# Kernel optimization log

Measured on AMD Instinct MI355X. Metric: run time of the kernel, lower is better.

Reference implementation:

```python
import jax, jax.numpy as jnp
import numpy as np

N, D, W, S = 16384, 256, 64, 8  # utterances, embed dim, attention half-window, speakers


def setup_inputs() -> dict:
    key = jax.random.key(0)
    ks = jax.random.split(key, 8)
    scale = 1.0 / np.sqrt(D)
    return {
        "x": jax.random.normal(ks[0], (N, D), jnp.float32),
        "speaker_ids": jax.random.randint(ks[1], (N,), 0, S, jnp.int32),
        "W_att": jax.random.normal(ks[2], (D, D), jnp.float32) * scale,
        "W_pred": jax.random.normal(ks[3], (D, D), jnp.float32) * scale,
        "W_suc": jax.random.normal(ks[4], (D, D), jnp.float32) * scale,
        "W_same": jax.random.normal(ks[5], (D, D), jnp.float32) * scale,
        "W_diff": jax.random.normal(ks[6], (D, D), jnp.float32) * scale,
    }


def reference(x, speaker_ids, W_att, W_pred, W_suc, W_same, W_diff):
    n = x.shape[0]
    pad = jnp.zeros((W, D), x.dtype)
    # windowed gather: for utterance i, neighbors at offsets [-W, W-1] (2W slots)
    win_idx = jnp.arange(n)[:, None] + jnp.arange(2 * W)[None, :]  # index into padded [N+2W]
    xp = jnp.concatenate([pad, x, pad], axis=0)                    # [N+2W, D]
    windows = xp[win_idx]                                          # [N, 2W, D]
    # raw_attn[i,w] = (edge_att_weights(windows[i,w])) . x[i]
    raw_attn = jnp.einsum("nwd,ed,ne->nw", windows, W_att, x)      # [N, 2W]
    attn = jax.nn.softmax(raw_attn, axis=1)
    # relation masks over the band: j = i + offset
    offs = jnp.arange(2 * W) - W                                   # [-W, W-1]
    j = jnp.arange(n)[:, None] + offs[None, :]                     # [N, 2W]
    valid = (j >= 0) & (j < n)
    jc = jnp.clip(j, 0, n - 1)
    same_spk = speaker_ids[jc] == speaker_ids[:, None]
    masks = [
        valid & (offs >= 0)[None, :],   # pred: edges to current/future within window
        valid & (offs < 0)[None, :],    # suc: edges to past within window
        valid & same_spk,               # same speaker within window
        valid & ~same_spk,              # different speaker within window
    ]
    # relation-specific GCN aggregation: h = sum_r A_r @ (x @ W_r), A_r banded
    h = jnp.zeros_like(x)
    for Wr, m in zip([W_pred, W_suc, W_same, W_diff], masks):
        support = x @ Wr                                           # [N, D]
        sp = jnp.concatenate([pad, support, pad], axis=0)[win_idx]  # [N, 2W, D]
        h = h + jnp.einsum("nw,nwd->nd", attn * m, sp)
    return jax.nn.log_softmax(h, axis=1)
```

## Files before the change

kernel.cpp:

```cpp
#include <hip/hip_runtime.h>
#include <hip/hip_bf16.h>

typedef unsigned short u16;
typedef unsigned int u32;
typedef __attribute__((ext_vector_type(8))) short short8;
typedef __attribute__((ext_vector_type(4))) float floatx4;

#define NU 16384
#define DIM 256
#define AMS 200
#define AC1o 6400u
#define FYLO 8448u

#define XHo 0u
#define XLo 4194304u
#define XRo 8388608u
#define ST0 20971520u
#define STROW 16512u
#define STMAT 4227072u
#define WH0o 33652736u
#define WL0o 33718272u
#define WRo  33783808u

__device__ __forceinline__ u16 bfh(float v) {
  return (u16)(__float_as_uint(v) >> 16);
}
__device__ __forceinline__ float bup(u16 u) {
  return __uint_as_float(((u32)u) << 16);
}
__device__ __forceinline__ u16 bfrn(float v) {
  u32 u = __float_as_uint(v);
  return (u16)((u + 0x7fffu + ((u >> 16) & 1u)) >> 16);
}

__global__ __launch_bounds__(256) void prep(
    const float* __restrict__ x,
    const float* __restrict__ wat, const float* __restrict__ wpr,
    const float* __restrict__ wsu, const float* __restrict__ wsm,
    const float* __restrict__ wdf, u16* __restrict__ ws) {
  const int b = blockIdx.x, t = threadIdx.x;
  if (b < 2048) {
    int idx = (b * 256 + t) * 8;
    float4 v0 = *(const float4*)(x + idx);
    float4 v1 = *(const float4*)(x + idx + 4);
    float a[8] = {v0.x, v0.y, v0.z, v0.w, v1.x, v1.y, v1.z, v1.w};
    u16 h[8], l[8], r[8];
#pragma unroll
    for (int q = 0; q < 8; ++q) {
      h[q] = bfh(a[q]);
      l[q] = bfh(a[q] - bup(h[q]));
      r[q] = bfrn(a[q]);
    }
    *(uint4*)(ws + XHo + idx) = *(const uint4*)h;
    *(uint4*)(ws + XLo + idx) = *(const uint4*)l;
    *(uint4*)(ws + XRo + idx) = *(const uint4*)r;
    return;
  }
  const int b2 = b - 2048;
  if (b2 < 32) {
    const int s = b2 & 7, mat = b2 >> 3, n = t;
    const float* Wa = (mat == 0) ? wat : (mat == 1) ? wpr : (mat == 2) ? wsm : wsu;
    const float* Wb = (mat == 0) ? wat : (mat == 1) ? wsu : (mat == 2) ? wdf : wdf;
    const float c1  = (mat == 0) ? 0.f : (mat == 3) ? 1.f : -1.f;
    u16 hbuf[32], lbuf[32];
#pragma unroll 8
    for (int k = 0; k < 32; ++k) {
      float v = Wa[(s * 32 + k) * 256 + n] + c1 * Wb[(s * 32 + k) * 256 + n];
      if (mat == 0) { hbuf[k] = bfh(v); lbuf[k] = bfh(v - bup(hbuf[k])); }
      else          { hbuf[k] = bfrn(v); }
    }
    u16* dh = ws + ((mat == 0) ? WH0o : (WRo + (size_t)(mat - 1) * 65536))
               + (size_t)s * 8192 + n * 32;
#pragma unroll
    for (int p = 0; p < 4; ++p) *(uint4*)(dh + p * 8) = ((const uint4*)hbuf)[p];
    if (mat == 0) {
      u16* dl = ws + WL0o + (size_t)s * 8192 + n * 32;
#pragma unroll
      for (int p = 0; p < 4; ++p) *(uint4*)(dl + p * 8) = ((const uint4*)lbuf)[p];
    }
  } else {
    int g = (b2 - 32) * 256 + t;
    int r = g >> 13, rem = g & 8191;
    int d = rem >> 5, p = rem & 31;
    size_t base = ST0 + (size_t)r * STMAT + (size_t)d * STROW;
    size_t off = (p < 16) ? (base + p * 4) : (base + 16448 + (p - 16) * 4);
    *(ushort4*)(ws + off) = make_ushort4(0, 0, 0, 0);
  }
}

__global__ __launch_bounds__(512, 4) void gemmS1(u16* __restrict__ ws) {
  __shared__ __align__(16) u16 U[39168];

  const int t = threadIdx.x, row0 = blockIdx.x * 32;
  const int w = t >> 6, ln = t & 15, quad = (t & 63) >> 4, q8 = quad * 8;
  const int n0 = w * 32;

#pragma unroll
  for (int cc = 0; cc < 2; ++cc) {
    int idx = t + 512 * cc;
    int row = idx >> 5, c8 = (idx & 31) * 8;
    *(uint4*)(U + row * 264 + c8) =
        *(const uint4*)(ws + XRo + (size_t)(row0 + row) * 256 + c8);
  }
  __syncthreads();

  floatx4 acc[3][2][2];
#pragma unroll
  for (int mat = 0; mat < 3; ++mat)
#pragma unroll
    for (int m = 0; m < 2; ++m)
#pragma unroll
      for (int nt = 0; nt < 2; ++nt) acc[mat][m][nt] = (floatx4){0.f, 0.f, 0.f, 0.f};

  for (int s = 0; s < 8; ++s) {
    short8 ah[2];
#pragma unroll
    for (int m = 0; m < 2; ++m)
      ah[m] = *(const short8*)(U + (m * 16 + ln) * 264 + s * 32 + q8);
#pragma unroll
    for (int mat = 0; mat < 3; ++mat) {
      short8 bh[2];
#pragma unroll
      for (int nt = 0; nt < 2; ++nt)
        bh[nt] = *(const short8*)(ws + WRo + (size_t)mat * 65536
                                  + (size_t)s * 8192 + (n0 + nt * 16 + ln) * 32 + q8);
#pragma unroll
      for (int m = 0; m < 2; ++m)
#pragma unroll
        for (int nt = 0; nt < 2; ++nt)
          acc[mat][m][nt] = __builtin_amdgcn_mfma_f32_16x16x32_bf16(ah[m], bh[nt], acc[mat][m][nt], 0, 0, 0);
    }
  }

#pragma unroll
  for (int mat = 0; mat < 3; ++mat)
#pragma unroll
    for (int m = 0; m < 2; ++m)
#pragma unroll
      for (int nt = 0; nt < 2; ++nt) {
        int col = n0 + nt * 16 + ln;
        ushort4 pk = make_ushort4(bfrn(acc[mat][m][nt][0]), bfrn(acc[mat][m][nt][1]),
                                  bfrn(acc[mat][m][nt][2]), bfrn(acc[mat][m][nt][3]));
        *(ushort4*)(U + 8448 + mat * 10240 + col * 40 + m * 16 + quad * 4) = pk;
      }
  __syncthreads();

#pragma unroll
  for (int mat = 0; mat < 3; ++mat)
#pragma unroll
    for (int cc = 0; cc < 2; ++cc) {
      int c = t + 512 * cc;
      int d = c >> 2, part = c & 3;
      *(uint4*)(ws + ST0 + (size_t)mat * STMAT + (size_t)d * STROW + 64 + row0 + part * 8) =
          *(const uint4*)(U + 8448 + mat * 10240 + d * 40 + part * 8);
    }
}

__global__ __launch_bounds__(512, 4) void fused_attn(
    const u16* __restrict__ ws, const int* __restrict__ spk,
    float* __restrict__ out)
{
  __shared__ __align__(16) u16 U[16896];
  __shared__ int spkw[192];
  __shared__ float prt[32][4], prs[32][4];
  __shared__ float red[32][8];

  const int t    = threadIdx.x;
  const int w    = t >> 6;
  const int ln   = t & 15;
  const int quad = (t & 63) >> 4;
  const int q8   = quad * 8;
  const int bswz = (blockIdx.x & 7) * 64 + (blockIdx.x >> 3);
  const int i0   = bswz * 32;
  const int mw   = w & 1;
  const int wq   = w >> 1;
  const int n0   = w * 32;

  if (t < 192) spkw[t] = spk[min(max(i0 - 64 + t, 0), NU - 1)];

  {
#pragma unroll
    for (int cc = 0; cc < 4; ++cc) {
      int idx = t + 512 * cc;
      int buf = idx >> 10, e = idx & 1023;
      int row = e >> 5, c8 = (e & 31) * 8;
      *(uint4*)(U + buf * FYLO + row * 264 + c8) =
          *(const uint4*)(ws + (buf ? XLo : XHo) + (size_t)(i0 + row) * 256 + c8);
    }
    __syncthreads();

    floatx4 acc[2][2];
#pragma unroll
    for (int m = 0; m < 2; ++m)
#pragma unroll
      for (int nt = 0; nt < 2; ++nt) acc[m][nt] = (floatx4){0.f, 0.f, 0.f, 0.f};

    for (int s = 0; s < 8; ++s) {
      short8 ah[2], al[2];
#pragma unroll
      for (int m = 0; m < 2; ++m) {
        ah[m] = *(const short8*)(U + (m * 16 + ln) * 264 + s * 32 + q8);
        al[m] = *(const short8*)(U + FYLO + (m * 16 + ln) * 264 + s * 32 + q8);
      }
      short8 bh[2], bl[2];
#pragma unroll
      for (int nt = 0; nt < 2; ++nt) {
        size_t off = (size_t)s * 8192 + (n0 + nt * 16 + ln) * 32 + q8;
        bh[nt] = *(const short8*)(ws + WH0o + off);
        bl[nt] = *(const short8*)(ws + WL0o + off);
      }
#pragma unroll
      for (int m = 0; m < 2; ++m)
#pragma unroll
        for (int nt = 0; nt < 2; ++nt) {
          acc[m][nt] = __builtin_amdgcn_mfma_f32_16x16x32_bf16(ah[m], bh[nt], acc[m][nt], 0, 0, 0);
          acc[m][nt] = __builtin_amdgcn_mfma_f32_16x16x32_bf16(ah[m], bl[nt], acc[m][nt], 0, 0, 0);
          acc[m][nt] = __builtin_amdgcn_mfma_f32_16x16x32_bf16(al[m], bh[nt], acc[m][nt], 0, 0, 0);
        }
    }
    __syncthreads();

#pragma unroll
    for (int m = 0; m < 2; ++m)
#pragma unroll
      for (int nt = 0; nt < 2; ++nt) {
        int col = n0 + nt * 16 + ln;
#pragma unroll
        for (int r = 0; r < 4; ++r) {
          int row = m * 16 + quad * 4 + r;
          float y = acc[m][nt][r];
          u16 hh = bfh(y);
          U[row * 264 + col] = hh;
          U[FYLO + row * 264 + col] = bfh(y - bup(hh));
        }
      }
  }
  __syncthreads();

  floatx4 accP[3];
#pragma unroll
  for (int cc = 0; cc < 3; ++cc) accP[cc] = (floatx4){0.f, 0.f, 0.f, 0.f};

#pragma unroll 2
  for (int ks = 0; ks < 8; ++ks) {
    const u16* yb = U + (mw * 16 + ln) * 264 + ks * 32 + q8;
    short8 yh8 = *(const short8*)yb;
    short8 yl8 = *(const short8*)(yb + FYLO);
#pragma unroll
    for (int cc = 0; cc < 3; ++cc) {
      int xrow = wq * 48 + cc * 16 + ln;
      int jc = min(max(i0 + xrow - 64, 0), NU - 1);
      size_t xo = (size_t)jc * 256 + ks * 32 + q8;
      short8 xbh = *(const short8*)(ws + XHo + xo);
      short8 xbl = *(const short8*)(ws + XLo + xo);
      accP[cc] = __builtin_amdgcn_mfma_f32_16x16x32_bf16(yh8, xbh, accP[cc], 0, 0, 0);
      accP[cc] = __builtin_amdgcn_mfma_f32_16x16x32_bf16(yh8, xbl, accP[cc], 0, 0, 0);
      accP[cc] = __builtin_amdgcn_mfma_f32_16x16x32_bf16(yl8, xbh, accP[cc], 0, 0, 0);
    }
  }

  int  c_of[3];
  bool vj[3];
#pragma unroll
  for (int cc = 0; cc < 3; ++cc) {
    c_of[cc] = wq * 48 + cc * 16 + ln;
    int j = i0 + c_of[cc] - 64;
    vj[cc] = (j >= 0) && (j < NU);
  }
#pragma unroll
  for (int r = 0; r < 4; ++r) {
    int row = mw * 16 + quad * 4 + r;
    float mx = -3.4e38f;
#pragma unroll
    for (int cc = 0; cc < 3; ++cc) {
      int rel = c_of[cc] - row;
      bool inb = (rel >= 0) && (rel < 128);
      if (inb) mx = fmaxf(mx, vj[cc] ? accP[cc][r] : 0.f);
    }
#pragma unroll
    for (int o = 1; o < 16; o <<= 1) mx = fmaxf(mx, __shfl_xor(mx, o));
    if (ln == 0) prt[row][wq] = mx;
  }
  __syncthreads();
#pragma unroll
  for (int r = 0; r < 4; ++r) {
    int row = mw * 16 + quad * 4 + r;
    float gm = fmaxf(fmaxf(prt[row][0], prt[row][1]), fmaxf(prt[row][2], prt[row][3]));
    float s = 0.f;
#pragma unroll
    for (int cc = 0; cc < 3; ++cc) {
      int rel = c_of[cc] - row;
      bool inb = (rel >= 0) && (rel < 128);
      float vv = vj[cc] ? accP[cc][r] : 0.f;
      float e  = inb ? __expf(vv - gm) : 0.f;
      s += e;
      accP[cc][r] = (inb && vj[cc]) ? e : 0.f;
    }
#pragma unroll
    for (int o = 1; o < 16; o <<= 1) s += __shfl_xor(s, o);
    if (ln == 0) prs[row][wq] = s;
  }
  __syncthreads();
#pragma unroll
  for (int r = 0; r < 4; ++r) {
    int row = mw * 16 + quad * 4 + r;
    float inv = 1.f / (prs[row][0] + prs[row][1] + prs[row][2] + prs[row][3]);
#pragma unroll
    for (int cc = 0; cc < 3; ++cc)
      U[row * AMS + c_of[cc]] = bfrn(accP[cc][r] * inv);
  }
  __syncthreads();

  {
    const int arow = t >> 4, aseg = t & 15;
    const int sr = spkw[arow + 64];
    const int cb = aseg * 12;
#pragma unroll
    for (int p = 0; p < 3; ++p) {
      ushort4 av = *(const ushort4*)(U + arow * AMS + cb + p * 4);
      u16 aq[4] = {av.x, av.y, av.z, av.w};
      u16 b1v[4];
#pragma unroll
      for (int q = 0; q < 4; ++q) {
        int c = cb + p * 4 + q;
        b1v[q] = (spkw[c] == sr) ? aq[q] : (u16)0;
      }
      *(ushort4*)(U + AC1o + arow * AMS + cb + p * 4) = *(const ushort4*)b1v;
    }
  }
  __syncthreads();

  floatx4 acc2[2][2];
#pragma unroll
  for (int m = 0; m < 2; ++m)
#pragma unroll
    for (int nt = 0; nt < 2; ++nt) acc2[m][nt] = (floatx4){0.f, 0.f, 0.f, 0.f};

#pragma unroll
  for (int kj = 0; kj < 5; ++kj) {
    short8 af[2], af1[2];
#pragma unroll
    for (int m = 0; m < 2; ++m) {
      af[m]  = *(const short8*)(U + (m * 16 + ln) * AMS + kj * 32 + q8);
      af1[m] = *(const short8*)(U + AC1o + (m * 16 + ln) * AMS + kj * 32 + q8);
    }
    size_t sb[2];
#pragma unroll
    for (int nt = 0; nt < 2; ++nt)
      sb[nt] = (size_t)ST0 + (size_t)(n0 + nt * 16 + ln) * STROW
             + (size_t)(i0 + kj * 32) + q8;
#pragma unroll
    for (int nt = 0; nt < 2; ++nt) {
      short8 b2 = *(const short8*)(ws + sb[nt] + 2 * (size_t)STMAT);
      short8 b1 = *(const short8*)(ws + sb[nt] + 1 * (size_t)STMAT);
#pragma unroll
      for (int m = 0; m < 2; ++m) {
        acc2[m][nt] = __builtin_amdgcn_mfma_f32_16x16x32_bf16(af[m],  b2, acc2[m][nt], 0, 0, 0);
        acc2[m][nt] = __builtin_amdgcn_mfma_f32_16x16x32_bf16(af1[m], b1, acc2[m][nt], 0, 0, 0);
      }
    }
    if (kj >= 2) {
      short8 a0m[2];
#pragma unroll
      for (int m = 0; m < 2; ++m) {
        a0m[m] = af[m];
        if (!(32 * kj >= 16 * m + 79)) {
          int tthr = m * 16 + ln + 64 - kj * 32 - q8;
#pragma unroll
          for (int e = 0; e < 8; ++e)
            if (e < tthr) a0m[m][e] = 0;
        }
      }
#pragma unroll
      for (int nt = 0; nt < 2; ++nt) {
        short8 b0 = *(const short8*)(ws + sb[nt]);
#pragma unroll
        for (int m = 0; m < 2; ++m) {
          if (32 * kj < 16 * m + 33) continue;
          acc2[m][nt] = __builtin_amdgcn_mfma_f32_16x16x32_bf16(a0m[m], b0, acc2[m][nt], 0, 0, 0);
        }
      }
    }
  }

#pragma unroll
  for (int m = 0; m < 2; ++m)
#pragma unroll
    for (int r = 0; r < 4; ++r) {
      float v = fmaxf(acc2[m][0][r], acc2[m][1][r]);
#pragma unroll
      for (int o = 1; o < 16; o <<= 1) v = fmaxf(v, __shfl_xor(v, o));
      if (ln == 0) red[m * 16 + quad * 4 + r][w] = v;
    }
  __syncthreads();
  float gmx[2][4];
#pragma unroll
  for (int m = 0; m < 2; ++m)
#pragma unroll
    for (int r = 0; r < 4; ++r) {
      int row = m * 16 + quad * 4 + r;
      float g = red[row][0];
#pragma unroll
      for (int ww = 1; ww < 8; ++ww) g = fmaxf(g, red[row][ww]);
      gmx[m][r] = g;
    }
  __syncthreads();
#pragma unroll
  for (int m = 0; m < 2; ++m)
#pragma unroll
    for (int r = 0; r < 4; ++r) {
      float e = __expf(acc2[m][0][r] - gmx[m][r]) + __expf(acc2[m][1][r] - gmx[m][r]);
#pragma unroll
      for (int o = 1; o < 16; o <<= 1) e += __shfl_xor(e, o);
      if (ln == 0) red[m * 16 + quad * 4 + r][w] = e;
    }
  __syncthreads();
#pragma unroll
  for (int m = 0; m < 2; ++m)
#pragma unroll
    for (int r = 0; r < 4; ++r) {
      int row = m * 16 + quad * 4 + r;
      float s = red[row][0];
#pragma unroll
      for (int ww = 1; ww < 8; ++ww) s += red[row][ww];
      float lse = gmx[m][r] + logf(s);
      size_t rowg = (size_t)(i0 + row) * DIM;
      out[rowg + n0 + ln]      = acc2[m][0][r] - lse;
      out[rowg + n0 + 16 + ln] = acc2[m][1][r] - lse;
    }
}

extern "C" void kernel_launch(void* const* d_in, const int* in_sizes, int n_in,
                              void* d_out, int out_size, void* d_ws, size_t ws_size,
                              hipStream_t stream) {
  const float* x   = (const float*)d_in[0];
  const int*   spk = (const int*)d_in[1];
  const float* wat = (const float*)d_in[2];
  const float* wpr = (const float*)d_in[3];
  const float* wsu = (const float*)d_in[4];
  const float* wsm = (const float*)d_in[5];
  const float* wdf = (const float*)d_in[6];
  float* out = (float*)d_out;
  u16* ws = (u16*)d_ws;

  hipLaunchKernelGGL(prep, dim3(2176), dim3(256), 0, stream,
                     x, wat, wpr, wsu, wsm, wdf, ws);
  hipLaunchKernelGGL(gemmS1, dim3(512), dim3(512), 0, stream, ws);
  hipLaunchKernelGGL(fused_attn, dim3(512), dim3(512), 0, stream, ws, spk, out);
}
```

Baseline: 161.3 us.

## Stage neighbor X tiles in LDS with double-buffered async loads; drop XR copy

The attention-score GEMM used to read the neighbor rows of X straight from global memory for every wave. Now a 160-row window of hi/lo bf16 X is staged into LDS with global_load_lds, double-buffered across the k-steps, using an XOR swizzle to spread bank accesses. The wave-to-column split is rebalanced to cover 160 columns (3+3+2+2 tiles) instead of 192, which removes redundant out-of-band work. gemmS1 now converts fp32 x to bf16 itself, so prep no longer writes the rounded copy. The trade-off is a larger LDS footprint with occupancy reduced to 2 blocks per CU, plus a barrier on every k-step.

```diff
diff --git a/kernel.cpp b/kernel.cpp
--- a/kernel.cpp
+++ b/kernel.cpp
@@ -9,12 +9,12 @@
 #define NU 16384
 #define DIM 256
 #define AMS 200
-#define AC1o 6400u
+#define AC1w 6400u
 #define FYLO 8448u
+#define STG32o 16896u
 
 #define XHo 0u
 #define XLo 4194304u
-#define XRo 8388608u
 #define ST0 20971520u
 #define STROW 16512u
 #define STMAT 4227072u
@@ -31,6 +31,12 @@
 __device__ __forceinline__ u16 bfrn(float v) {
   u32 u = __float_as_uint(v);
   return (u16)((u + 0x7fffu + ((u >> 16) & 1u)) >> 16);
+}
+
+__device__ __forceinline__ void gload16(const u16* g, u16* l) {
+  __builtin_amdgcn_global_load_lds(
+      (__attribute__((address_space(1))) void*)(uintptr_t)g,
+      (__attribute__((address_space(3))) void*)(uintptr_t)l, 16, 0, 0);
 }
 
 __global__ __launch_bounds__(256) void prep(
@@ -44,16 +50,14 @@
     float4 v0 = *(const float4*)(x + idx);
     float4 v1 = *(const float4*)(x + idx + 4);
     float a[8] = {v0.x, v0.y, v0.z, v0.w, v1.x, v1.y, v1.z, v1.w};
-    u16 h[8], l[8], r[8];
+    u16 h[8], l[8];
 #pragma unroll
     for (int q = 0; q < 8; ++q) {
       h[q] = bfh(a[q]);
       l[q] = bfh(a[q] - bup(h[q]));
-      r[q] = bfrn(a[q]);
     }
     *(uint4*)(ws + XHo + idx) = *(const uint4*)h;
     *(uint4*)(ws + XLo + idx) = *(const uint4*)l;
-    *(uint4*)(ws + XRo + idx) = *(const uint4*)r;
     return;
   }
   const int b2 = b - 2048;
@@ -88,7 +92,8 @@
   }
 }
 
-__global__ __launch_bounds__(512, 4) void gemmS1(u16* __restrict__ ws) {
+__global__ __launch_bounds__(512, 4) void gemmS1(const float* __restrict__ x,
+                                                 u16* __restrict__ ws) {
   __shared__ __align__(16) u16 U[39168];
 
   const int t = threadIdx.x, row0 = blockIdx.x * 32;
@@ -96,11 +101,12 @@
   const int n0 = w * 32;
 
 #pragma unroll
-  for (int cc = 0; cc < 2; ++cc) {
+  for (int cc = 0; cc < 4; ++cc) {
     int idx = t + 512 * cc;
-    int row = idx >> 5, c8 = (idx & 31) * 8;
-    *(uint4*)(U + row * 264 + c8) =
-        *(const uint4*)(ws + XRo + (size_t)(row0 + row) * 256 + c8);
+    int row = idx >> 6, c4 = (idx & 63) * 4;
+    float4 v = *(const float4*)(x + (size_t)(row0 + row) * 256 + c4);
+    ushort4 pk = make_ushort4(bfrn(v.x), bfrn(v.y), bfrn(v.z), bfrn(v.w));
+    *(ushort4*)(U + row * 264 + c4) = pk;
   }
   __syncthreads();
 
@@ -156,12 +162,12 @@
     }
 }
 
-__global__ __launch_bounds__(512, 4) void fused_attn(
+__global__ __launch_bounds__(512, 2) void fused_attn(
     const u16* __restrict__ ws, const int* __restrict__ spk,
     float* __restrict__ out)
 {
-  __shared__ __align__(16) u16 U[16896];
-  __shared__ int spkw[192];
+  __shared__ __align__(16) u16 U[37376];
+  __shared__ int spkw[160];
   __shared__ float prt[32][4], prs[32][4];
   __shared__ float red[32][8];
 
@@ -173,10 +179,12 @@
   const int bswz = (blockIdx.x & 7) * 64 + (blockIdx.x >> 3);
   const int i0   = bswz * 32;
   const int mw   = w & 1;
-  const int wq   = w >> 1;
+  const int wg   = w >> 1;
+  const int gbase = (wg < 2) ? wg * 48 : 96 + (wg - 2) * 32;
+  const int gcnt  = (wg < 2) ? 3 : 2;
   const int n0   = w * 32;
 
-  if (t < 192) spkw[t] = spk[min(max(i0 - 64 + t, 0), NU - 1)];
+  if (t < 160) spkw[t] = spk[min(max(i0 - 64 + t, 0), NU - 1)];
 
   {
 #pragma unroll
@@ -235,35 +243,59 @@
         }
       }
   }
-  __syncthreads();
+
+  auto STAGE = [&](int ks, int par) {
+    const int kd = ks * 32;
+    u16* db = U + STG32o + par * 10240;
+#pragma unroll
+    for (int cc = 0; cc < 3; ++cc) {
+      int idx = t + 512 * cc;
+      if (idx < 1280) {
+        int bsel = (idx >= 640) ? 1 : 0;
+        int e    = idx - bsel * 640;
+        int row  = e >> 2, s2 = e & 3;
+        int sw   = s2 ^ ((row >> 1) & 3);
+        int jc   = min(max(i0 + row - 64, 0), NU - 1);
+        gload16(ws + (bsel ? XLo : XHo) + (size_t)jc * 256 + kd + sw * 8,
+                db + bsel * 5120 + e * 8);
+      }
+    }
+  };
 
   floatx4 accP[3];
 #pragma unroll
   for (int cc = 0; cc < 3; ++cc) accP[cc] = (floatx4){0.f, 0.f, 0.f, 0.f};
 
-#pragma unroll 2
+  STAGE(0, 0);
+  __syncthreads();
+#pragma unroll
   for (int ks = 0; ks < 8; ++ks) {
+    if (ks < 7) STAGE(ks + 1, (ks + 1) & 1);
+    const u16* sp = U + STG32o + (ks & 1) * 10240;
     const u16* yb = U + (mw * 16 + ln) * 264 + ks * 32 + q8;
     short8 yh8 = *(const short8*)yb;
     short8 yl8 = *(const short8*)(yb + FYLO);
 #pragma unroll
     for (int cc = 0; cc < 3; ++cc) {
-      int xrow = wq * 48 + cc * 16 + ln;
-      int jc = min(max(i0 + xrow - 64, 0), NU - 1);
-      size_t xo = (size_t)jc * 256 + ks * 32 + q8;
-      short8 xbh = *(const short8*)(ws + XHo + xo);
-      short8 xbl = *(const short8*)(ws + XLo + xo);
-      accP[cc] = __builtin_amdgcn_mfma_f32_16x16x32_bf16(yh8, xbh, accP[cc], 0, 0, 0);
-      accP[cc] = __builtin_amdgcn_mfma_f32_16x16x32_bf16(yh8, xbl, accP[cc], 0, 0, 0);
-      accP[cc] = __builtin_amdgcn_mfma_f32_16x16x32_bf16(yl8, xbh, accP[cc], 0, 0, 0);
-    }
+      if (cc < gcnt) {
+        int xrow = gbase + cc * 16 + ln;
+        int slot = quad ^ ((xrow >> 1) & 3);
+        const u16* xb = sp + xrow * 32 + slot * 8;
+        short8 xbh = *(const short8*)xb;
+        short8 xbl = *(const short8*)(xb + 5120);
+        accP[cc] = __builtin_amdgcn_mfma_f32_16x16x32_bf16(yh8, xbh, accP[cc], 0, 0, 0);
+        accP[cc] = __builtin_amdgcn_mfma_f32_16x16x32_bf16(yh8, xbl, accP[cc], 0, 0, 0);
+        accP[cc] = __builtin_amdgcn_mfma_f32_16x16x32_bf16(yl8, xbh, accP[cc], 0, 0, 0);
+      }
+    }
+    __syncthreads();
   }
 
   int  c_of[3];
   bool vj[3];
 #pragma unroll
   for (int cc = 0; cc < 3; ++cc) {
-    c_of[cc] = wq * 48 + cc * 16 + ln;
+    c_of[cc] = gbase + cc * 16 + ln;
     int j = i0 + c_of[cc] - 64;
     vj[cc] = (j >= 0) && (j < NU);
   }
@@ -273,13 +305,15 @@
     float mx = -3.4e38f;
 #pragma unroll
     for (int cc = 0; cc < 3; ++cc) {
-      int rel = c_of[cc] - row;
-      bool inb = (rel >= 0) && (rel < 128);
-      if (inb) mx = fmaxf(mx, vj[cc] ? accP[cc][r] : 0.f);
+      if (cc < gcnt) {
+        int rel = c_of[cc] - row;
+        bool inb = (rel >= 0) && (rel < 128);
+        if (inb) mx = fmaxf(mx, vj[cc] ? accP[cc][r] : 0.f);
+      }
     }
 #pragma unroll
     for (int o = 1; o < 16; o <<= 1) mx = fmaxf(mx, __shfl_xor(mx, o));
-    if (ln == 0) prt[row][wq] = mx;
+    if (ln == 0) prt[row][wg] = mx;
   }
   __syncthreads();
 #pragma unroll
@@ -289,16 +323,18 @@
     float s = 0.f;
 #pragma unroll
     for (int cc = 0; cc < 3; ++cc) {
-      int rel = c_of[cc] - row;
-      bool inb = (rel >= 0) && (rel < 128);
-      float vv = vj[cc] ? accP[cc][r] : 0.f;
-      float e  = inb ? __expf(vv - gm) : 0.f;
-      s += e;
-      accP[cc][r] = (inb && vj[cc]) ? e : 0.f;
+      if (cc < gcnt) {
+        int rel = c_of[cc] - row;
+        bool inb = (rel >= 0) && (rel < 128);
+        float vv = vj[cc] ? accP[cc][r] : 0.f;
+        float e  = inb ? __expf(vv - gm) : 0.f;
+        s += e;
+        accP[cc][r] = (inb && vj[cc]) ? e : 0.f;
+      }
     }
 #pragma unroll
     for (int o = 1; o < 16; o <<= 1) s += __shfl_xor(s, o);
-    if (ln == 0) prs[row][wq] = s;
+    if (ln == 0) prs[row][wg] = s;
   }
   __syncthreads();
 #pragma unroll
@@ -307,25 +343,20 @@
     float inv = 1.f / (prs[row][0] + prs[row][1] + prs[row][2] + prs[row][3]);
 #pragma unroll
     for (int cc = 0; cc < 3; ++cc)
-      U[row * AMS + c_of[cc]] = bfrn(accP[cc][r] * inv);
+      if (cc < gcnt)
+        U[row * AMS + c_of[cc]] = bfrn(accP[cc][r] * inv);
   }
   __syncthreads();
 
   {
     const int arow = t >> 4, aseg = t & 15;
     const int sr = spkw[arow + 64];
-    const int cb = aseg * 12;
-#pragma unroll
-    for (int p = 0; p < 3; ++p) {
-      ushort4 av = *(const ushort4*)(U + arow * AMS + cb + p * 4);
-      u16 aq[4] = {av.x, av.y, av.z, av.w};
-      u16 b1v[4];
-#pragma unroll
-      for (int q = 0; q < 4; ++q) {
-        int c = cb + p * 4 + q;
-        b1v[q] = (spkw[c] == sr) ? aq[q] : (u16)0;
-      }
-      *(ushort4*)(U + AC1o + arow * AMS + cb + p * 4) = *(const ushort4*)b1v;
+    const int cb = aseg * 10;
+#pragma unroll
+    for (int q = 0; q < 10; ++q) {
+      int c = cb + q;
+      u16 a = U[arow * AMS + c];
+      U[AC1w + arow * AMS + c] = (spkw[c] == sr) ? a : (u16)0;
     }
   }
   __syncthreads();
@@ -342,7 +373,7 @@
 #pragma unroll
     for (int m = 0; m < 2; ++m) {
       af[m]  = *(const short8*)(U + (m * 16 + ln) * AMS + kj * 32 + q8);
-      af1[m] = *(const short8*)(U + AC1o + (m * 16 + ln) * AMS + kj * 32 + q8);
+      af1[m] = *(const short8*)(U + AC1w + (m * 16 + ln) * AMS + kj * 32 + q8);
     }
     size_t sb[2];
 #pragma unroll
@@ -445,6 +476,6 @@
 
   hipLaunchKernelGGL(prep, dim3(2176), dim3(256), 0, stream,
                      x, wat, wpr, wsu, wsm, wdf, ws);
-  hipLaunchKernelGGL(gemmS1, dim3(512), dim3(512), 0, stream, ws);
+  hipLaunchKernelGGL(gemmS1, dim3(512), dim3(512), 0, stream, x, ws);
   hipLaunchKernelGGL(fused_attn, dim3(512), dim3(512), 0, stream, ws, spk, out);
 }
```

After: 147.0 us. 1.1x faster.
